# Kernel optimization log

Measured on AMD Instinct MI355X. Metric: run time of the kernel, lower is better.

## Reference

```python
import jax, jax.numpy as jnp
import numpy as np

EMBED = 1024
N_HEADS = 16
HEAD_DIM = EMBED // N_HEADS
B, T = 2, 2048


def setup_inputs() -> dict:
    key = jax.random.key(0)
    k1, k2, k3 = jax.random.split(key, 3)
    x = jax.random.normal(k1, (B, T, EMBED), dtype=jnp.float32)
    # torch nn.Linear(embed, 3*embed, bias=False): weight [3C, C]; store as [C, 3C] for x @ W
    w_attn = jax.random.normal(k2, (EMBED, 3 * EMBED), dtype=jnp.float32) * (EMBED ** -0.5)
    w_proj = jax.random.normal(k3, (EMBED, EMBED), dtype=jnp.float32) * (EMBED ** -0.5)
    return {"x": x, "w_attn": w_attn, "w_proj": w_proj}


def reference(x, w_attn, w_proj):
    Bb, Tt, C = x.shape
    kqv = x @ w_attn  # [B, T, 3C]
    # NOTE: original code unpacks as k, q, v (k first)
    k, q, v = jnp.split(kqv, 3, axis=2)
    def heads(t):
        return t.reshape(Bb, Tt, N_HEADS, HEAD_DIM).transpose(0, 2, 1, 3)  # [B, H, T, D]
    k, q, v = heads(k), heads(q), heads(v)
    scale = HEAD_DIM ** -0.5
    wei = jnp.einsum("bhqd,bhkd->bhqk", q, k) * scale  # [B, H, T, T]
    mask = jnp.tril(jnp.ones((Tt, Tt), dtype=bool))
    wei = jnp.where(mask[None, None], wei, -jnp.inf)
    wei = jax.nn.softmax(wei, axis=-1)
    y = jnp.einsum("bhqk,bhkd->bhqd", wei, v)  # [B, H, T, D]
    y = y.transpose(0, 2, 1, 3).reshape(Bb, Tt, C)
    return y @ w_proj
```

## Files before the change

kernel.cpp:

```cpp
#include <hip/hip_runtime.h>

typedef unsigned short u16;
typedef unsigned int u32;

typedef __attribute__((ext_vector_type(4))) float f32x4;
typedef __attribute__((ext_vector_type(8))) short s16x8;
typedef __attribute__((ext_vector_type(4))) u32 u32x4;

__device__ __forceinline__ u16 f2bf(float f) {
    u32 u = __builtin_bit_cast(u32, f);
    u += 0x7fffu + ((u >> 16) & 1u);
    return (u16)(u >> 16);
}

__device__ __forceinline__ u32 pk_bf16(float a, float b) {
    return (u32)f2bf(a) | ((u32)f2bf(b) << 16);
}

__device__ __forceinline__ u32 cvtpk(float a, float b) {
    u32 r;
    asm("v_cvt_pk_bf16_f32 %0, %1, %2" : "=v"(r) : "v"(a), "v"(b));
    return r;
}

__device__ __forceinline__ float bf2f(u16 h) {
    u32 u = ((u32)h) << 16;
    return __builtin_bit_cast(float, u);
}

__device__ __forceinline__ void pl32swap(u32& a, u32& b) {
    asm volatile("v_permlane32_swap_b32 %0, %1" : "+v"(a), "+v"(b));
}
__device__ __forceinline__ void pl16swap(u32& a, u32& b) {
    asm volatile("v_permlane16_swap_b32 %0, %1" : "+v"(a), "+v"(b));
}

#define EXP2(x) exp2f(x)

__device__ __forceinline__ void gload16(const u16* g, u16* l) {
    __builtin_amdgcn_global_load_lds(
        (const __attribute__((address_space(1))) void*)(const void*)g,
        (__attribute__((address_space(3))) void*)(void*)l, 16, 0, 0);
}

__global__ void k_cast(const float* __restrict__ in, u16* __restrict__ out) {
    int i = (blockIdx.x * 256 + threadIdx.x) * 4;
    float4 v = *(const float4*)(in + i);
    uint2 pk;
    pk.x = pk_bf16(v.x, v.y);
    pk.y = pk_bf16(v.z, v.w);
    *(uint2*)(out + i) = pk;
}

__global__ void k_transpose(const float* __restrict__ in, u16* __restrict__ out,
                            int K, int N) {
    __shared__ float tile[32][33];
    int n0 = blockIdx.x * 32, k0 = blockIdx.y * 32;
    int x = threadIdx.x, y = threadIdx.y;
#pragma unroll
    for (int j = 0; j < 32; j += 8)
        tile[y + j][x] = in[(size_t)(k0 + y + j) * N + n0 + x];
    __syncthreads();
#pragma unroll
    for (int j = 0; j < 32; j += 8)
        out[(size_t)(n0 + y + j) * K + k0 + x] = f2bf(tile[x][y + j]);
}

template <int EPI>
__global__ __launch_bounds__(256, 2) void k_gemm(
        const u16* __restrict__ A, const u16* __restrict__ Bt,
        void* __restrict__ Cout, u16* __restrict__ Vt, int N, int K) {
    __shared__ u16 As[128 * 32];
    __shared__ u16 Bs[128 * 32];
    const int nbn = N >> 7;
    const int cpx = (int)gridDim.x >> 3;
    const int bid = (int)blockIdx.x;
    const int swb = (bid & 7) * cpx + (bid >> 3);
    const int bm = swb / nbn, bn = swb % nbn;
    const int tid = threadIdx.x;
    const int wv = tid >> 6, ln = tid & 63;
    const int lg = ln >> 4, lr = ln & 15;
    const int wr = (wv >> 1) << 6, wc = (wv & 1) << 6;

    const u16* gA = A + (size_t)(bm * 128 + wv * 32 + (ln >> 2)) * K + (ln & 3) * 8;
    const u16* gB = Bt + (size_t)(bn * 128 + wv * 32 + (ln >> 2)) * K + (ln & 3) * 8;
    u16* lA = As + wv * 1024;
    u16* lB = Bs + wv * 1024;

    f32x4 acc[4][4] = {};

    for (int k0 = 0; k0 < K; k0 += 32) {
        gload16(gA + k0, lA);
        gload16(gA + k0 + 16 * K, lA + 512);
        gload16(gB + k0, lB);
        gload16(gB + k0 + 16 * K, lB + 512);
        __syncthreads();
        s16x8 af[4], bf[4];
#pragma unroll
        for (int mi = 0; mi < 4; ++mi)
            af[mi] = *(const s16x8*)&As[(wr + mi * 16 + lr) * 32 + lg * 8];
#pragma unroll
        for (int ni = 0; ni < 4; ++ni)
            bf[ni] = *(const s16x8*)&Bs[(wc + ni * 16 + lr) * 32 + lg * 8];
#pragma unroll
        for (int mi = 0; mi < 4; ++mi)
#pragma unroll
            for (int ni = 0; ni < 4; ++ni)
                acc[mi][ni] = __builtin_amdgcn_mfma_f32_16x16x32_bf16(
                        af[mi], bf[ni], acc[mi][ni], 0, 0, 0);
        __syncthreads();
    }

    const int crow0 = bm * 128 + wr + lg * 4;
    const int ccol0 = bn * 128 + wc + lr;
    if (EPI == 0) {
        float* Co = (float*)Cout;
#pragma unroll
        for (int mi = 0; mi < 4; ++mi)
#pragma unroll
            for (int ni = 0; ni < 4; ++ni)
#pragma unroll
                for (int r = 0; r < 4; ++r)
                    Co[(size_t)(crow0 + mi * 16 + r) * N + ccol0 + ni * 16] =
                            acc[mi][ni][r];
    } else {
        if (bn < 16) {
            const float qs = (bn >= 8) ? 0.18033688011112042f : 1.0f;
            u16* Co = (u16*)Cout;
#pragma unroll
            for (int mi = 0; mi < 4; ++mi)
#pragma unroll
                for (int ni = 0; ni < 4; ++ni)
#pragma unroll
                    for (int r = 0; r < 4; ++r)
                        Co[(size_t)(crow0 + mi * 16 + r) * 3072 + ccol0 + ni * 16] =
                                f2bf(acc[mi][ni][r] * qs);
        } else {
#pragma unroll
            for (int mi = 0; mi < 4; ++mi) {
                int row = crow0 + mi * 16;
                int bb = row >> 11, t = row & 2047;
#pragma unroll
                for (int ni = 0; ni < 4; ++ni) {
                    int hd = ccol0 + ni * 16 - 2048;
                    uint2 pk;
                    pk.x = pk_bf16(acc[mi][ni][0], acc[mi][ni][1]);
                    pk.y = pk_bf16(acc[mi][ni][2], acc[mi][ni][3]);
                    *(uint2*)&Vt[(size_t)(bb * 1024 + hd) * 2048 + t] = pk;
                }
            }
        }
    }
}

__global__ __launch_bounds__(512, 4) void k_attn(
        const u16* __restrict__ kqv, const u16* __restrict__ Vt,
        u16* __restrict__ y) {
    const int orig = blockIdx.x;
    const int xcd = orig & 7, slot = orig >> 3;
    const int bh = xcd * 4 + (slot >> 4);
    const int pr = slot & 15;
    const int b = bh >> 4, h = bh & 15;
    const int tid = threadIdx.x;
    const int wave = tid >> 6;
    const int g = wave >> 2;
    const int wv4 = wave & 3;
    const int lane = tid & 63;
    const int lg = lane >> 4, lr = lane & 15;

    __shared__ u16 Ks[2][2][64 * 64];
    __shared__ u16 Vs[2][2][64 * 64];
    __shared__ u16 comb[4 * 64 * 20];

    const u16* Kg = kqv + (size_t)b * 2048 * 3072 + h * 64;
    const u16* Qg = Kg + 1024;
    const u16* Vg = Vt + (size_t)bh * 64 * 2048;

    const int srow = wv4 * 16 + (lane >> 3);
    const int cK = (lane & 7) ^ (lane >> 3);
    const u16* kg0 = Kg + (size_t)srow * 3072 + cK * 8;
    const u16* vg0 = Vg + (size_t)srow * 2048 + cK * 8;
    const int swz = lr & 7;

    s16x8 ones;
#pragma unroll
    for (int i = 0; i < 8; ++i) ones[i] = (short)0x3F80;

#define STAGE(bb, t)                                      \
    {                                                     \
        const u16* kp_ = kg0 + (size_t)(t) * 64 * 3072;   \
        const u16* vp_ = vg0 + (size_t)(t) * 64;          \
        u16* lk_ = &Ks[g][bb][wv4 * 1024];                \
        u16* lv_ = &Vs[g][bb][wv4 * 1024];                \
        gload16(kp_, lk_);                                \
        gload16(kp_ + 8 * 3072, lk_ + 512);               \
        gload16(vp_, lv_);                                \
        gload16(vp_ + 8 * 2048, lv_ + 512);               \
    }

    for (int pass = 0; pass < 2; ++pass) {
        const int qt = pass ? (31 - pr) : pr;
        const int nkt = qt + 1;
        const int iters = (nkt + 1) >> 1;
        const int qbase = qt * 64 + wv4 * 16;

        const u16* qrp = Qg + (size_t)(qbase + lr) * 3072;
        const s16x8 qf0 = *(const s16x8*)(qrp + lg * 8);
        const s16x8 qf1 = *(const s16x8*)(qrp + 32 + lg * 8);

        f32x4 o[4] = {};
        f32x4 l4 = {};

        if (g < nkt) STAGE(0, g);
        asm volatile("s_waitcnt vmcnt(0)\n\ts_barrier" ::: "memory");

        for (int i = 0; i < iters; ++i) {
            const int cur = i & 1;
            const int t = 2 * i + g;
            if (t + 2 < nkt) STAGE(cur ^ 1, t + 2);
            if (t < nkt) {
                f32x4 st[4];
                __builtin_amdgcn_s_setprio(1);
#pragma unroll
                for (int kb = 0; kb < 4; ++kb) {
                    const int row = kb * 16 + lr;
                    s16x8 kf0 = *(const s16x8*)&Ks[g][cur][row * 64 + ((lg ^ swz) << 3)];
                    s16x8 kf1 = *(const s16x8*)&Ks[g][cur][row * 64 + (((4 + lg) ^ swz) << 3)];
                    f32x4 z = {};
                    z = __builtin_amdgcn_mfma_f32_16x16x32_bf16(kf0, qf0, z, 0, 0, 0);
                    z = __builtin_amdgcn_mfma_f32_16x16x32_bf16(kf1, qf1, z, 0, 0, 0);
                    st[kb] = z;
                }
                __builtin_amdgcn_s_setprio(0);

                if (t == nkt - 1) {
                    const int q_abs = qbase + lr;
                    const int kb0 = t * 64 + lg * 4;
#pragma unroll
                    for (int kb = 0; kb < 4; ++kb)
#pragma unroll
                        for (int r = 0; r < 4; ++r)
                            st[kb][r] = EXP2((kb0 + kb * 16 + r <= q_abs)
                                                 ? st[kb][r] : -3e38f);
                } else {
#pragma unroll
                    for (int kb = 0; kb < 4; ++kb)
#pragma unroll
                        for (int r = 0; r < 4; ++r) st[kb][r] = EXP2(st[kb][r]);
                }

                u32 E[2][2], O[2][2];
#pragma unroll
                for (int kbh = 0; kbh < 2; ++kbh)
#pragma unroll
                    for (int hh = 0; hh < 2; ++hh) {
                        E[kbh][hh] = cvtpk(st[2 * kbh][2 * hh], st[2 * kbh][2 * hh + 1]);
                        O[kbh][hh] = cvtpk(st[2 * kbh + 1][2 * hh], st[2 * kbh + 1][2 * hh + 1]);
                    }
#pragma unroll
                for (int kbh = 0; kbh < 2; ++kbh)
#pragma unroll
                    for (int hh = 0; hh < 2; ++hh) {
                        pl32swap(E[kbh][hh], O[kbh][hh]);
                        pl16swap(E[kbh][hh], O[kbh][hh]);
                    }

                __builtin_amdgcn_s_setprio(1);
#pragma unroll
                for (int half = 0; half < 2; ++half) {
                    u32x4 pw;
                    pw.x = E[half][0];
                    pw.y = E[half][1];
                    pw.z = O[half][0];
                    pw.w = O[half][1];
                    s16x8 pf = __builtin_bit_cast(s16x8, pw);
                    l4 = __builtin_amdgcn_mfma_f32_16x16x32_bf16(ones, pf, l4, 0, 0, 0);
#pragma unroll
                    for (int dt = 0; dt < 4; ++dt) {
                        const int vrow = dt * 16 + lr;
                        s16x8 vf = *(const s16x8*)&Vs[g][cur][vrow * 64 +
                                                    (((half * 4 + lg) ^ swz) << 3)];
                        o[dt] = __builtin_amdgcn_mfma_f32_16x16x32_bf16(vf, pf, o[dt], 0, 0, 0);
                    }
                }
                __builtin_amdgcn_s_setprio(0);
            }
            asm volatile("s_waitcnt vmcnt(0)\n\ts_barrier" ::: "memory");
        }

        if (g == 1) {
            u16* ce = comb + (size_t)(wv4 * 64 + lane) * 20;
#pragma unroll
            for (int dt = 0; dt < 4; ++dt) {
                uint2 w;
                w.x = cvtpk(o[dt][0], o[dt][1]);
                w.y = cvtpk(o[dt][2], o[dt][3]);
                *(uint2*)(ce + dt * 4) = w;
            }
            *(float*)(ce + 16) = l4[0];
        }
        __syncthreads();
        if (g == 0) {
            const u16* ce = comb + (size_t)(wv4 * 64 + lane) * 20;
            float l = l4[0] + *(const float*)(ce + 16);
#pragma unroll
            for (int dt = 0; dt < 4; ++dt) {
                uint2 w = *(const uint2*)(ce + dt * 4);
                o[dt][0] += bf2f((u16)(w.x & 0xffff));
                o[dt][1] += bf2f((u16)(w.x >> 16));
                o[dt][2] += bf2f((u16)(w.y & 0xffff));
                o[dt][3] += bf2f((u16)(w.y >> 16));
            }
            const float inv = 1.0f / l;
            u16* yb = y + (size_t)(b * 2048 + qbase + lr) * 1024 + h * 64;
#pragma unroll
            for (int dt = 0; dt < 4; ++dt) {
                uint2 w;
                w.x = cvtpk(o[dt][0] * inv, o[dt][1] * inv);
                w.y = cvtpk(o[dt][2] * inv, o[dt][3] * inv);
                *(uint2*)(yb + dt * 16 + lg * 4) = w;
            }
        }
        __syncthreads();
    }
#undef STAGE
}

extern "C" void kernel_launch(void* const* d_in, const int* in_sizes, int n_in,
                              void* d_out, int out_size, void* d_ws, size_t ws_size,
                              hipStream_t stream) {
    const float* x = (const float*)d_in[0];
    const float* w_attn = (const float*)d_in[1];
    const float* w_proj = (const float*)d_in[2];
    float* out = (float*)d_out;
    char* ws = (char*)d_ws;

    u16* x_bf = (u16*)(ws);
    u16* wat  = (u16*)(ws + (size_t)(8 << 20));
    u16* wpt  = (u16*)(ws + (size_t)(14 << 20));
    u16* kqv  = (u16*)(ws + (size_t)(16 << 20));
    u16* vt   = (u16*)(ws + (size_t)(40 << 20));
    u16* yb   = (u16*)(ws + (size_t)(48 << 20));

    k_cast<<<4096, 256, 0, stream>>>(x, x_bf);
    k_transpose<<<dim3(96, 32), dim3(32, 8), 0, stream>>>(w_attn, wat, 1024, 3072);
    k_transpose<<<dim3(32, 32), dim3(32, 8), 0, stream>>>(w_proj, wpt, 1024, 1024);
    k_gemm<1><<<32 * 24, 256, 0, stream>>>(x_bf, wat, kqv, vt, 3072, 1024);
    k_attn<<<512, 512, 0, stream>>>(kqv, vt, yb);
    k_gemm<0><<<32 * 8, 256, 0, stream>>>(yb, wpt, out, nullptr, 1024, 1024);
}
```

Baseline: 172.0 us.

## Halve attention KV tile to 32 keys and fuse prep kernels into one launch

The attention kernel now stages 32-key K/V tiles instead of 64, with new swizzles for the narrower V tile. The comb buffer is aliased onto V shared memory, cutting LDS use from about 74KB to 32KB per block, which allows more resident blocks and shrinks per-iteration register state. The cast and two transpose kernels are merged into one launch to save launch overhead. The cost is twice as many loop iterations and barriers per query tile, plus masking that now covers the last two subtiles.

```diff
diff --git a/kernel.cpp b/kernel.cpp
--- a/kernel.cpp
+++ b/kernel.cpp
@@ -43,27 +43,41 @@
         (__attribute__((address_space(3))) void*)(void*)l, 16, 0, 0);
 }
 
-__global__ void k_cast(const float* __restrict__ in, u16* __restrict__ out) {
-    int i = (blockIdx.x * 256 + threadIdx.x) * 4;
-    float4 v = *(const float4*)(in + i);
-    uint2 pk;
-    pk.x = pk_bf16(v.x, v.y);
-    pk.y = pk_bf16(v.z, v.w);
-    *(uint2*)(out + i) = pk;
-}
-
-__global__ void k_transpose(const float* __restrict__ in, u16* __restrict__ out,
-                            int K, int N) {
+__global__ void k_prep(const float* __restrict__ x, u16* __restrict__ x_bf,
+                       const float* __restrict__ wa, u16* __restrict__ wat,
+                       const float* __restrict__ wp, u16* __restrict__ wpt) {
+    const int bid = blockIdx.x;
+    const int tid = threadIdx.x;
+    if (bid < 4096) {
+        int i = (bid * 256 + tid) * 4;
+        float4 v = *(const float4*)(x + i);
+        uint2 pk;
+        pk.x = pk_bf16(v.x, v.y);
+        pk.y = pk_bf16(v.z, v.w);
+        *(uint2*)(x_bf + i) = pk;
+        return;
+    }
+    const float* in;
+    u16* out;
+    int n0, k0, N;
+    if (bid < 4096 + 3072) {
+        int loc = bid - 4096;
+        in = wa; out = wat; N = 3072;
+        n0 = (loc % 96) * 32; k0 = (loc / 96) * 32;
+    } else {
+        int loc = bid - 4096 - 3072;
+        in = wp; out = wpt; N = 1024;
+        n0 = (loc & 31) * 32; k0 = (loc >> 5) * 32;
+    }
     __shared__ float tile[32][33];
-    int n0 = blockIdx.x * 32, k0 = blockIdx.y * 32;
-    int x = threadIdx.x, y = threadIdx.y;
+    const int tx = tid & 31, ty = tid >> 5;
 #pragma unroll
     for (int j = 0; j < 32; j += 8)
-        tile[y + j][x] = in[(size_t)(k0 + y + j) * N + n0 + x];
+        tile[ty + j][tx] = in[(size_t)(k0 + ty + j) * N + n0 + tx];
     __syncthreads();
 #pragma unroll
     for (int j = 0; j < 32; j += 8)
-        out[(size_t)(n0 + y + j) * K + k0 + x] = f2bf(tile[x][y + j]);
+        out[(size_t)(n0 + ty + j) * 1024 + k0 + tx] = f2bf(tile[tx][ty + j]);
 }
 
 template <int EPI>
@@ -168,40 +182,38 @@
     const int lane = tid & 63;
     const int lg = lane >> 4, lr = lane & 15;
 
-    __shared__ u16 Ks[2][2][64 * 64];
-    __shared__ u16 Vs[2][2][64 * 64];
-    __shared__ u16 comb[4 * 64 * 20];
+    __shared__ u16 smem[16384];
+    u16* const KsB = smem;
+    u16* const VsB = smem + 8192;
+    u16* const comb = VsB;
 
     const u16* Kg = kqv + (size_t)b * 2048 * 3072 + h * 64;
     const u16* Qg = Kg + 1024;
     const u16* Vg = Vt + (size_t)bh * 64 * 2048;
 
-    const int srow = wv4 * 16 + (lane >> 3);
-    const int cK = (lane & 7) ^ (lane >> 3);
-    const u16* kg0 = Kg + (size_t)srow * 3072 + cK * 8;
-    const u16* vg0 = Vg + (size_t)srow * 2048 + cK * 8;
-    const int swz = lr & 7;
+    const u16* kg0 = Kg + (size_t)(wv4 * 8 + (lane >> 3)) * 3072 +
+                     (((lane & 7) ^ (lane >> 3)) << 3);
+    const u16* vg0 = Vg + (size_t)(wv4 * 16 + (lane >> 2)) * 2048 +
+                     (((lane & 3) ^ ((lane >> 3) & 3)) << 3);
+    const int swzK = lr & 7;
+    const int swzV = (lr >> 1) & 3;
 
     s16x8 ones;
 #pragma unroll
     for (int i = 0; i < 8; ++i) ones[i] = (short)0x3F80;
 
-#define STAGE(bb, t)                                      \
-    {                                                     \
-        const u16* kp_ = kg0 + (size_t)(t) * 64 * 3072;   \
-        const u16* vp_ = vg0 + (size_t)(t) * 64;          \
-        u16* lk_ = &Ks[g][bb][wv4 * 1024];                \
-        u16* lv_ = &Vs[g][bb][wv4 * 1024];                \
-        gload16(kp_, lk_);                                \
-        gload16(kp_ + 8 * 3072, lk_ + 512);               \
-        gload16(vp_, lv_);                                \
-        gload16(vp_ + 8 * 2048, lv_ + 512);               \
+#define STAGE(bb, t)                                        \
+    {                                                       \
+        gload16(kg0 + (size_t)(t) * 32 * 3072,              \
+                KsB + (g * 2 + (bb)) * 2048 + wv4 * 512);   \
+        gload16(vg0 + (size_t)(t) * 32,                     \
+                VsB + (g * 2 + (bb)) * 2048 + wv4 * 512);   \
     }
 
     for (int pass = 0; pass < 2; ++pass) {
         const int qt = pass ? (31 - pr) : pr;
-        const int nkt = qt + 1;
-        const int iters = (nkt + 1) >> 1;
+        const int nkt = 2 * (qt + 1);
+        const int iters = qt + 1;
         const int qbase = qt * 64 + wv4 * 16;
 
         const u16* qrp = Qg + (size_t)(qbase + lr) * 3072;
@@ -211,80 +223,68 @@
         f32x4 o[4] = {};
         f32x4 l4 = {};
 
-        if (g < nkt) STAGE(0, g);
+        STAGE(0, g);
         asm volatile("s_waitcnt vmcnt(0)\n\ts_barrier" ::: "memory");
 
         for (int i = 0; i < iters; ++i) {
             const int cur = i & 1;
             const int t = 2 * i + g;
-            if (t + 2 < nkt) STAGE(cur ^ 1, t + 2);
-            if (t < nkt) {
-                f32x4 st[4];
-                __builtin_amdgcn_s_setprio(1);
-#pragma unroll
-                for (int kb = 0; kb < 4; ++kb) {
-                    const int row = kb * 16 + lr;
-                    s16x8 kf0 = *(const s16x8*)&Ks[g][cur][row * 64 + ((lg ^ swz) << 3)];
-                    s16x8 kf1 = *(const s16x8*)&Ks[g][cur][row * 64 + (((4 + lg) ^ swz) << 3)];
-                    f32x4 z = {};
-                    z = __builtin_amdgcn_mfma_f32_16x16x32_bf16(kf0, qf0, z, 0, 0, 0);
-                    z = __builtin_amdgcn_mfma_f32_16x16x32_bf16(kf1, qf1, z, 0, 0, 0);
-                    st[kb] = z;
-                }
-                __builtin_amdgcn_s_setprio(0);
-
-                if (t == nkt - 1) {
-                    const int q_abs = qbase + lr;
-                    const int kb0 = t * 64 + lg * 4;
-#pragma unroll
-                    for (int kb = 0; kb < 4; ++kb)
-#pragma unroll
-                        for (int r = 0; r < 4; ++r)
-                            st[kb][r] = EXP2((kb0 + kb * 16 + r <= q_abs)
-                                                 ? st[kb][r] : -3e38f);
-                } else {
-#pragma unroll
-                    for (int kb = 0; kb < 4; ++kb)
-#pragma unroll
-                        for (int r = 0; r < 4; ++r) st[kb][r] = EXP2(st[kb][r]);
-                }
-
-                u32 E[2][2], O[2][2];
-#pragma unroll
-                for (int kbh = 0; kbh < 2; ++kbh)
-#pragma unroll
-                    for (int hh = 0; hh < 2; ++hh) {
-                        E[kbh][hh] = cvtpk(st[2 * kbh][2 * hh], st[2 * kbh][2 * hh + 1]);
-                        O[kbh][hh] = cvtpk(st[2 * kbh + 1][2 * hh], st[2 * kbh + 1][2 * hh + 1]);
-                    }
-#pragma unroll
-                for (int kbh = 0; kbh < 2; ++kbh)
-#pragma unroll
-                    for (int hh = 0; hh < 2; ++hh) {
-                        pl32swap(E[kbh][hh], O[kbh][hh]);
-                        pl16swap(E[kbh][hh], O[kbh][hh]);
-                    }
-
-                __builtin_amdgcn_s_setprio(1);
-#pragma unroll
-                for (int half = 0; half < 2; ++half) {
-                    u32x4 pw;
-                    pw.x = E[half][0];
-                    pw.y = E[half][1];
-                    pw.z = O[half][0];
-                    pw.w = O[half][1];
-                    s16x8 pf = __builtin_bit_cast(s16x8, pw);
-                    l4 = __builtin_amdgcn_mfma_f32_16x16x32_bf16(ones, pf, l4, 0, 0, 0);
-#pragma unroll
-                    for (int dt = 0; dt < 4; ++dt) {
-                        const int vrow = dt * 16 + lr;
-                        s16x8 vf = *(const s16x8*)&Vs[g][cur][vrow * 64 +
-                                                    (((half * 4 + lg) ^ swz) << 3)];
-                        o[dt] = __builtin_amdgcn_mfma_f32_16x16x32_bf16(vf, pf, o[dt], 0, 0, 0);
-                    }
-                }
-                __builtin_amdgcn_s_setprio(0);
-            }
+            if (i + 1 < iters) STAGE(cur ^ 1, t + 2);
+            const u16* Kc = KsB + (g * 2 + cur) * 2048;
+            const u16* Vc = VsB + (g * 2 + cur) * 2048;
+
+            f32x4 st[2];
+            __builtin_amdgcn_s_setprio(1);
+#pragma unroll
+            for (int kb = 0; kb < 2; ++kb) {
+                const int row = kb * 16 + lr;
+                s16x8 kf0 = *(const s16x8*)&Kc[row * 64 + ((lg ^ swzK) << 3)];
+                s16x8 kf1 = *(const s16x8*)&Kc[row * 64 + (((4 + lg) ^ swzK) << 3)];
+                f32x4 z = {};
+                z = __builtin_amdgcn_mfma_f32_16x16x32_bf16(kf0, qf0, z, 0, 0, 0);
+                z = __builtin_amdgcn_mfma_f32_16x16x32_bf16(kf1, qf1, z, 0, 0, 0);
+                st[kb] = z;
+            }
+            __builtin_amdgcn_s_setprio(0);
+
+            if (t >= nkt - 2) {
+                const int q_abs = qbase + lr;
+                const int kb0 = t * 32 + lg * 4;
+#pragma unroll
+                for (int kb = 0; kb < 2; ++kb)
+#pragma unroll
+                    for (int r = 0; r < 4; ++r)
+                        st[kb][r] = EXP2((kb0 + kb * 16 + r <= q_abs)
+                                             ? st[kb][r] : -3e38f);
+            } else {
+#pragma unroll
+                for (int kb = 0; kb < 2; ++kb)
+#pragma unroll
+                    for (int r = 0; r < 4; ++r) st[kb][r] = EXP2(st[kb][r]);
+            }
+
+            u32 E[2], O[2];
+#pragma unroll
+            for (int hh = 0; hh < 2; ++hh) {
+                E[hh] = cvtpk(st[0][2 * hh], st[0][2 * hh + 1]);
+                O[hh] = cvtpk(st[1][2 * hh], st[1][2 * hh + 1]);
+                pl32swap(E[hh], O[hh]);
+                pl16swap(E[hh], O[hh]);
+            }
+            u32x4 pw;
+            pw.x = E[0]; pw.y = E[1]; pw.z = O[0]; pw.w = O[1];
+            s16x8 pf = __builtin_bit_cast(s16x8, pw);
+
+            __builtin_amdgcn_s_setprio(1);
+            l4 = __builtin_amdgcn_mfma_f32_16x16x32_bf16(ones, pf, l4, 0, 0, 0);
+#pragma unroll
+            for (int dt = 0; dt < 4; ++dt) {
+                const int vrow = dt * 16 + lr;
+                s16x8 vf = *(const s16x8*)&Vc[vrow * 32 + ((lg ^ swzV) << 3)];
+                o[dt] = __builtin_amdgcn_mfma_f32_16x16x32_bf16(vf, pf, o[dt], 0, 0, 0);
+            }
+            __builtin_amdgcn_s_setprio(0);
+
             asm volatile("s_waitcnt vmcnt(0)\n\ts_barrier" ::: "memory");
         }
 
@@ -342,9 +342,8 @@
     u16* vt   = (u16*)(ws + (size_t)(40 << 20));
     u16* yb   = (u16*)(ws + (size_t)(48 << 20));
 
-    k_cast<<<4096, 256, 0, stream>>>(x, x_bf);
-    k_transpose<<<dim3(96, 32), dim3(32, 8), 0, stream>>>(w_attn, wat, 1024, 3072);
-    k_transpose<<<dim3(32, 32), dim3(32, 8), 0, stream>>>(w_proj, wpt, 1024, 1024);
+    k_prep<<<4096 + 3072 + 1024, 256, 0, stream>>>(x, x_bf, w_attn, wat,
+                                                   w_proj, wpt);
     k_gemm<1><<<32 * 24, 256, 0, stream>>>(x_bf, wat, kqv, vt, 3072, 1024);
     k_attn<<<512, 512, 0, stream>>>(kqv, vt, yb);
     k_gemm<0><<<32 * 8, 256, 0, stream>>>(yb, wpt, out, nullptr, 1024, 1024);
```

After: 170.3 us. No clear change (-1.0%).
